# Kernel tuning notes

Hardware: AMD Instinct MI355X
Metric: run time of the kernel (lower is better)

Reference implementation:

```python
import jax, jax.numpy as jnp
import numpy as np

NEG_SLOPE = 0.2

def setup_inputs() -> dict:
    key = jax.random.key(0)
    k1, k2, k3, k4 = jax.random.split(key, 4)
    B, N, Fin, H, Fo = 8, 2000, 128, 4, 64
    x = jax.random.normal(k1, (B, N, Fin), dtype=jnp.float32)
    adj = jax.random.randint(k2, (N, N), 0, 2, dtype=jnp.int32)
    W = jax.random.normal(k3, (Fin, H * Fo), dtype=jnp.float32) * (1.0 / np.sqrt(Fin))
    a = jax.random.normal(k4, (H, 2 * Fo), dtype=jnp.float32) * 0.1
    return {"x": x, "adj": adj, "W": W, "a": a}

def reference(x, adj, W, a):
    B, N, _ = x.shape
    H, F2 = a.shape
    Fo = F2 // 2
    h = (x @ W).reshape(B, N, H, Fo)  # [B,N,H,Fo]
    # cat([h_i,h_j])*a summed over 2Fo decomposes into per-node src/dst scores
    a_src, a_dst = a[:, :Fo], a[:, Fo:]
    e_i = jnp.einsum('bnhf,hf->bnh', h, a_src)  # source (query) contribution
    e_j = jnp.einsum('bnhf,hf->bnh', h, a_dst)  # target (key) contribution
    e = jax.nn.leaky_relu(e_i[:, :, None, :] + e_j[:, None, :, :], NEG_SLOPE)  # [B,N,N,H]
    mask = (adj == 0)[None, :, :, None]
    e = jnp.where(mask, -jnp.inf, e)
    alpha = jax.nn.softmax(e, axis=2)  # softmax over neighbors j
    # dropout is identity in eval mode
    out = jnp.einsum('bijh,bjhf->bihf', alpha, h).mean(axis=2)  # [B,N,Fo]
    return out, alpha
```

## Files before the change

kernel.cpp:

```cpp
#include <hip/hip_runtime.h>
#include <math.h>

#define BB 8
#define NN 2000
#define FIN 128
#define HH 4
#define FO 64
#define CC 256

typedef short bf16x8 __attribute__((ext_vector_type(8)));
typedef float f32x4 __attribute__((ext_vector_type(4)));
typedef unsigned long long u64;

__device__ __forceinline__ unsigned short f2bf(float v) {
    union { float f; unsigned u; } x;
    x.f = v;
    unsigned r = x.u + 0x7fffu + ((x.u >> 16) & 1u);
    return (unsigned short)(r >> 16);
}

__global__ __launch_bounds__(256) void k_adjbits(const int* __restrict__ adj,
                                                 u64* __restrict__ adjb) {
    const int w = blockIdx.x * 4 + (threadIdx.x >> 6);
    const int lane = threadIdx.x & 63;
    const int i = w >> 5, wd = w & 31;
    const int j = wd * 64 + lane;
    int av = 0;
    if (j < NN) av = adj[(size_t)i * NN + j];
    const u64 mask = __ballot(av != 0);
    if (lane == 0) adjb[(size_t)i * 32 + wd] = mask;
}

__global__ __launch_bounds__(256) void k_gemm_fused(const float* __restrict__ x,
                                                    const float* __restrict__ W,
                                                    const float* __restrict__ a,
                                                    float* __restrict__ e_src,
                                                    float* __restrict__ e_dst,
                                                    unsigned short* __restrict__ hT) {
    __shared__ __align__(16) char smraw[8192];
    float* xs = (float*)smraw;
    unsigned short* sm = (unsigned short*)smraw;
    const int row0 = blockIdx.x * 16;
    const int t = threadIdx.x;
    for (int k = t; k < 16 * FIN; k += 256) xs[k] = x[row0 * FIN + k];
    __syncthreads();
    const int c = t;
    const int h = c >> 6, f = c & 63, lane = t & 63;
    float acc[16];
#pragma unroll
    for (int r = 0; r < 16; ++r) acc[r] = 0.f;
#pragma unroll 2
    for (int k = 0; k < FIN; k += 4) {
        const float w0 = W[(k + 0) * CC + c];
        const float w1 = W[(k + 1) * CC + c];
        const float w2 = W[(k + 2) * CC + c];
        const float w3 = W[(k + 3) * CC + c];
#pragma unroll
        for (int r = 0; r < 16; ++r) {
            const float4 xv = *(const float4*)(xs + r * FIN + k);
            acc[r] = fmaf(xv.x, w0, fmaf(xv.y, w1, fmaf(xv.z, w2, fmaf(xv.w, w3, acc[r]))));
        }
    }
    const int b = row0 / NN;
    const int n0 = row0 - b * NN;
    const float aS = a[h * 2 * FO + f];
    const float aD = a[h * 2 * FO + FO + f];
#pragma unroll
    for (int r = 0; r < 16; ++r) {
        float p1 = acc[r] * aS;
        float p2 = acc[r] * aD;
#pragma unroll
        for (int off = 32; off > 0; off >>= 1) {
            p1 += __shfl_xor(p1, off);
            p2 += __shfl_xor(p2, off);
        }
        if (lane == 0) {
            e_src[(b * HH + h) * NN + n0 + r] = p1;
            e_dst[(b * HH + h) * NN + n0 + r] = p2;
        }
    }
    __syncthreads();
#pragma unroll
    for (int r = 0; r < 16; ++r) sm[r * 256 + c] = f2bf(acc[r]);
    __syncthreads();
    const int s = n0 >> 5;
    const int qbase = (n0 >> 3) & 3;
    unsigned short* base = hT + (size_t)b * HH * 131072 + s * 2048;
#pragma unroll
    for (int it2 = 0; it2 < 2; ++it2) {
        const int k2 = it2 * 256 + t;
        const int hh = (k2 >> 7) & 3, ft2 = (k2 >> 5) & 3, l16 = (k2 >> 1) & 15, g = k2 & 1;
        const int col = hh * 64 + ft2 * 16 + l16;
        unsigned v[4];
#pragma unroll
        for (int p = 0; p < 4; ++p) {
            const unsigned lo = sm[(g * 8 + 2 * p) * 256 + col];
            const unsigned hi = sm[(g * 8 + 2 * p + 1) * 256 + col];
            v[p] = lo | (hi << 16);
        }
        uint4 pkt; pkt.x = v[0]; pkt.y = v[1]; pkt.z = v[2]; pkt.w = v[3];
        *(uint4*)(base + (size_t)hh * 131072 + ft2 * 512 + (qbase + g) * 128 + l16 * 8) = pkt;
    }
}

__global__ __launch_bounds__(256) void k_padT(unsigned short* __restrict__ hT) {
    const int k = blockIdx.x * 256 + threadIdx.x;
    const int bh = k / 384;
    const int r = k - bh * 384;
    const int ft = r / 96;
    const int c = r - ft * 96;
    size_t off;
    if (c < 32) off = 62 * 2048 + ft * 512 + 256 + c * 8;
    else        off = 63 * 2048 + ft * 512 + (size_t)(c - 32) * 8;
    uint4 z; z.x = 0; z.y = 0; z.z = 0; z.w = 0;
    *(uint4*)(hT + (size_t)bh * 131072 + off) = z;
}

__global__ __launch_bounds__(256) void k_softmax_l(const u64* __restrict__ adjb,
                                                   const float* __restrict__ e_src,
                                                   const float* __restrict__ e_dst,
                                                   float* __restrict__ rlArr) {
    const int widx = blockIdx.x * 4 + (threadIdx.x >> 6);
    const int lane = threadIdx.x & 63;
    const int b = widx / (NN * HH);
    const int rem = widx - b * (NN * HH);
    const int i = rem / HH;
    const int h = rem - i * HH;
    const float* ed = e_dst + (b * HH + h) * NN;
    const u64* ab = adjb + (size_t)i * 32;
    const float ei = e_src[(b * HH + h) * NN + i];
    float l = 0.f;
#pragma unroll 2
    for (int it = 0; it < 8; ++it) {
        const int j = it * 256 + lane * 4;
        const u64 wbits = ab[j >> 6];
        const unsigned nib = (unsigned)((wbits >> (j & 63)) & 0xFull);
        const float4 ev = *(const float4*)(ed + j);
        float s0 = ei + ev.x; s0 = s0 > 0.f ? s0 : 0.2f * s0;
        float s1 = ei + ev.y; s1 = s1 > 0.f ? s1 : 0.2f * s1;
        float s2 = ei + ev.z; s2 = s2 > 0.f ? s2 : 0.2f * s2;
        float s3 = ei + ev.w; s3 = s3 > 0.f ? s3 : 0.2f * s3;
        const float q0 = (nib & 1u) ? __expf(s0) : 0.f;
        const float q1 = (nib & 2u) ? __expf(s1) : 0.f;
        const float q2 = (nib & 4u) ? __expf(s2) : 0.f;
        const float q3 = (nib & 8u) ? __expf(s3) : 0.f;
        l += (q0 + q1) + (q2 + q3);
    }
#pragma unroll
    for (int off = 32; off > 0; off >>= 1) l += __shfl_xor(l, off);
    if (lane == 0) rlArr[(b * HH + h) * NN + i] = 1.f / l;
}

__global__ __launch_bounds__(512) void k_out_mfma4(const u64* __restrict__ adjb,
                                                   const unsigned short* __restrict__ hT,
                                                   const float* __restrict__ e_src,
                                                   const float* __restrict__ e_dst,
                                                   const float* __restrict__ rlArr,
                                                   float* __restrict__ out) {
    __shared__ float red[32][72];
    const int blk = blockIdx.x;
    const int b = blk / 63;
    const int it = blk - b * 63;
    const int t = threadIdx.x;
    const int w = t >> 6, lane = t & 63;
    const int h = w >> 1, half = w & 1;
    const int l16 = lane & 15, quad = lane >> 4;
    const int i = it * 32 + half * 16 + l16;
    const int ic = i < NN ? i : NN - 1;
    const int bh = b * HH + h;
    const float es = e_src[bh * NN + ic];
    const float rl = (i < NN) ? rlArr[bh * NN + ic] : 0.f;
    const float* ed = e_dst + bh * NN;
    const u64* ab = adjb + (size_t)ic * 32;
    const unsigned short* hbase = hT + (size_t)bh * 131072 + (size_t)lane * 8;

    f32x4 acc[4];
#pragma unroll
    for (int ft = 0; ft < 4; ++ft) {
        acc[ft][0] = 0.f; acc[ft][1] = 0.f; acc[ft][2] = 0.f; acc[ft][3] = 0.f;
    }

#pragma unroll 2
    for (int jt = 0; jt < 32; ++jt) {
        const int j0 = jt * 64;
        const u64 bits = ab[jt];
        const unsigned m0 = ((unsigned)(bits >> (quad * 8))) & 0xffu;
        const unsigned m1 = ((unsigned)(bits >> 32) >> (quad * 8)) & 0xffu;
        const float4 ea0 = *(const float4*)(ed + j0 + quad * 8);
        const float4 ea1 = *(const float4*)(ed + j0 + quad * 8 + 4);
        const float4 eb0 = *(const float4*)(ed + j0 + 32 + quad * 8);
        const float4 eb1 = *(const float4*)(ed + j0 + 32 + quad * 8 + 4);
        const unsigned short* hp0 = hbase + (size_t)jt * 4096;

        {
            const float ev[8] = {ea0.x, ea0.y, ea0.z, ea0.w, ea1.x, ea1.y, ea1.z, ea1.w};
            bf16x8 bfr;
#pragma unroll
            for (int e = 0; e < 8; ++e) {
                float s = es + ev[e];
                s = s > 0.f ? s : 0.2f * s;
                float p = __expf(s) * rl;
                p = ((m0 >> e) & 1u) ? p : 0.f;
                bfr[e] = (short)f2bf(p);
            }
#pragma unroll
            for (int ft = 0; ft < 4; ++ft) {
                const bf16x8 af = *(const bf16x8*)(hp0 + ft * 512);
                acc[ft] = __builtin_amdgcn_mfma_f32_16x16x32_bf16(af, bfr, acc[ft], 0, 0, 0);
            }
        }
        {
            const float ev[8] = {eb0.x, eb0.y, eb0.z, eb0.w, eb1.x, eb1.y, eb1.z, eb1.w};
            bf16x8 bfr;
#pragma unroll
            for (int e = 0; e < 8; ++e) {
                float s = es + ev[e];
                s = s > 0.f ? s : 0.2f * s;
                float p = __expf(s) * rl;
                p = ((m1 >> e) & 1u) ? p : 0.f;
                bfr[e] = (short)f2bf(p);
            }
#pragma unroll
            for (int ft = 0; ft < 4; ++ft) {
                const bf16x8 af = *(const bf16x8*)(hp0 + 2048 + ft * 512);
                acc[ft] = __builtin_amdgcn_mfma_f32_16x16x32_bf16(af, bfr, acc[ft], 0, 0, 0);
            }
        }
    }
#pragma unroll
    for (int ph = 0; ph < HH; ++ph) {
        if (h == ph) {
            if (ph == 0) {
#pragma unroll
                for (int ft = 0; ft < 4; ++ft)
                    *(f32x4*)(&red[half * 16 + l16][ft * 16 + quad * 4]) = acc[ft];
            } else {
#pragma unroll
                for (int ft = 0; ft < 4; ++ft) {
                    f32x4 cur = *(const f32x4*)(&red[half * 16 + l16][ft * 16 + quad * 4]);
#pragma unroll
                    for (int r = 0; r < 4; ++r) cur[r] += acc[ft][r];
                    *(f32x4*)(&red[half * 16 + l16][ft * 16 + quad * 4]) = cur;
                }
            }
        }
        __syncthreads();
    }
    const int ii = t >> 4, f4 = (t & 15) * 4;
    const int gi = it * 32 + ii;
    if (gi < NN) {
        const f32x4 v = *(const f32x4*)(&red[ii][f4]);
        f32x4 o;
#pragma unroll
        for (int r = 0; r < 4; ++r) o[r] = 0.25f * v[r];
        *(f32x4*)(out + (size_t)(b * NN + gi) * FO + f4) = o;
    }
}

__global__ __launch_bounds__(256) void k_alpha_bits(const u64* __restrict__ adjb,
                                                    const float* __restrict__ e_src,
                                                    const float* __restrict__ e_dst,
                                                    const float* __restrict__ rlArr,
                                                    float* __restrict__ alpha) {
    const int bi = blockIdx.x;
    const int b = bi / NN, i = bi - b * NN;
    const int t = threadIdx.x;
    float ei[HH], rr[HH];
#pragma unroll
    for (int h = 0; h < HH; ++h) {
        ei[h] = e_src[(b * HH + h) * NN + i];
        rr[h] = rlArr[(b * HH + h) * NN + i];
    }
    const float* ed = e_dst + b * HH * NN;
    const u64* ab = adjb + (size_t)i * 32;
    float* arow = alpha + (size_t)(b * NN + i) * (NN * HH);
    for (int jq = t; jq < NN / 4; jq += 256) {
        const int j0 = jq * 4;
        const unsigned bits4 = (unsigned)((ab[j0 >> 6] >> (j0 & 63)) & 0xFull);
        float e4[HH * 4];
#pragma unroll
        for (int h = 0; h < HH; ++h) {
            const float4 v = *(const float4*)(ed + h * NN + j0);
            e4[h * 4 + 0] = v.x; e4[h * 4 + 1] = v.y; e4[h * 4 + 2] = v.z; e4[h * 4 + 3] = v.w;
        }
#pragma unroll
        for (int jj = 0; jj < 4; ++jj) {
            const bool av = (bits4 >> jj) & 1u;
            float o[HH];
#pragma unroll
            for (int h = 0; h < HH; ++h) {
                float s = ei[h] + e4[h * 4 + jj];
                s = s > 0.f ? s : 0.2f * s;
                o[h] = av ? __expf(s) * rr[h] : 0.f;
            }
            float4 ov = {o[0], o[1], o[2], o[3]};
            *(float4*)(arow + (size_t)(j0 + jj) * HH) = ov;
        }
    }
}

__global__ __launch_bounds__(256) void k_alpha_adj(const int* __restrict__ adj,
                                                   const float* __restrict__ e_src,
                                                   const float* __restrict__ e_dst,
                                                   const float* __restrict__ rlArr,
                                                   float* __restrict__ alpha) {
    const int bi = blockIdx.x;
    const int b = bi / NN, i = bi - b * NN;
    const int t = threadIdx.x;
    float ei[HH], rr[HH];
#pragma unroll
    for (int h = 0; h < HH; ++h) {
        ei[h] = e_src[(b * HH + h) * NN + i];
        rr[h] = rlArr[(b * HH + h) * NN + i];
    }
    const float* ed = e_dst + b * HH * NN;
    const int* adjrow = adj + (size_t)i * NN;
    float* arow = alpha + (size_t)(b * NN + i) * (NN * HH);
    for (int jq = t; jq < NN / 4; jq += 256) {
        const int j0 = jq * 4;
        const int4 av4 = *(const int4*)(adjrow + j0);
        const int avs[4] = {av4.x, av4.y, av4.z, av4.w};
        float e4[HH * 4];
#pragma unroll
        for (int h = 0; h < HH; ++h) {
            const float4 v = *(const float4*)(ed + h * NN + j0);
            e4[h * 4 + 0] = v.x; e4[h * 4 + 1] = v.y; e4[h * 4 + 2] = v.z; e4[h * 4 + 3] = v.w;
        }
#pragma unroll
        for (int jj = 0; jj < 4; ++jj) {
            const bool av = avs[jj] != 0;
            float o[HH];
#pragma unroll
            for (int h = 0; h < HH; ++h) {
                float s = ei[h] + e4[h * 4 + jj];
                s = s > 0.f ? s : 0.2f * s;
                o[h] = av ? __expf(s) * rr[h] : 0.f;
            }
            float4 ov = {o[0], o[1], o[2], o[3]};
            *(float4*)(arow + (size_t)(j0 + jj) * HH) = ov;
        }
    }
}

extern "C" void kernel_launch(void* const* d_in, const int* in_sizes, int n_in,
                              void* d_out, int out_size, void* d_ws, size_t ws_size,
                              hipStream_t stream) {
    const float* x  = (const float*)d_in[0];
    const int* adj  = (const int*)d_in[1];
    const float* W  = (const float*)d_in[2];
    const float* a  = (const float*)d_in[3];

    float* out = (float*)d_out;
    float* alpha = out + (size_t)BB * NN * FO;

    unsigned short* hT = (unsigned short*)alpha;
    u64* adjb_scratch = (u64*)((char*)alpha + 8388608);

    char* ws = (char*)d_ws;
    float* e_src = (float*)ws;
    float* e_dst = (float*)(ws + 256000);
    float* rlArr = (float*)(ws + 512000);
    const bool ws_has_adjb = ws_size >= 1280000;
    u64* adjb = ws_has_adjb ? (u64*)(ws + 768000) : adjb_scratch;

    k_adjbits<<<16000, 256, 0, stream>>>(adj, adjb);
    k_gemm_fused<<<1000, 256, 0, stream>>>(x, W, a, e_src, e_dst, hT);
    k_padT<<<48, 256, 0, stream>>>(hT);
    k_softmax_l<<<16000, 256, 0, stream>>>(adjb, e_src, e_dst, rlArr);
    k_out_mfma4<<<504, 512, 0, stream>>>(adjb, hT, e_src, e_dst, rlArr, out);
    if (ws_has_adjb)
        k_alpha_bits<<<16000, 256, 0, stream>>>(adjb, e_src, e_dst, rlArr, alpha);
    else
        k_alpha_adj<<<16000, 256, 0, stream>>>(adj, e_src, e_dst, rlArr, alpha);
}
```

Baseline: 763.0 us.

## Fuse softmax denominator into MFMA aggregation kernel and merge adjacency/pad kernels

Removes the separate softmax row-sum kernel. The aggregation kernel now accumulates unnormalized exp weights, reduces the per-row sum across quads, rescales the accumulators and writes rlArr for the later alpha kernel. The adjacency bit-packing and hT padding kernels are merged into one launch with a grid-stride loop. The aggregation kernel also stages e_dst in shared memory, uses 256-thread blocks of 16 rows, and drops the bounds checks since 2000 divides by 16. This saves a pass over the adjacency bits and two launches. In exchange, bf16 rounding now applies to unnormalized exponentials, which could overflow or lose precision for large scores.

```diff
diff --git a/kernel.cpp b/kernel.cpp
--- a/kernel.cpp
+++ b/kernel.cpp
@@ -19,16 +19,31 @@
     return (unsigned short)(r >> 16);
 }
 
-__global__ __launch_bounds__(256) void k_adjbits(const int* __restrict__ adj,
-                                                 u64* __restrict__ adjb) {
-    const int w = blockIdx.x * 4 + (threadIdx.x >> 6);
-    const int lane = threadIdx.x & 63;
-    const int i = w >> 5, wd = w & 31;
-    const int j = wd * 64 + lane;
-    int av = 0;
-    if (j < NN) av = adj[(size_t)i * NN + j];
-    const u64 mask = __ballot(av != 0);
-    if (lane == 0) adjb[(size_t)i * 32 + wd] = mask;
+__global__ __launch_bounds__(256) void k_adjpad(const int* __restrict__ adj,
+                                                u64* __restrict__ adjb,
+                                                unsigned short* __restrict__ hT) {
+    if (blockIdx.x < 1000) {
+        const int lane = threadIdx.x & 63;
+        for (int w = blockIdx.x * 4 + (threadIdx.x >> 6); w < 64000; w += 4000) {
+            const int i = w >> 5, wd = w & 31;
+            const int j = wd * 64 + lane;
+            int av = 0;
+            if (j < NN) av = adj[(size_t)i * NN + j];
+            const u64 mask = __ballot(av != 0);
+            if (lane == 0) adjb[(size_t)i * 32 + wd] = mask;
+        }
+    } else {
+        const int k = (blockIdx.x - 1000) * 256 + threadIdx.x;
+        const int bh = k / 384;
+        const int r = k - bh * 384;
+        const int ft = r / 96;
+        const int c = r - ft * 96;
+        size_t off;
+        if (c < 32) off = 62 * 2048 + ft * 512 + 256 + c * 8;
+        else        off = 63 * 2048 + ft * 512 + (size_t)(c - 32) * 8;
+        uint4 z; z.x = 0; z.y = 0; z.z = 0; z.w = 0;
+        *(uint4*)(hT + (size_t)bh * 131072 + off) = z;
+    }
 }
 
 __global__ __launch_bounds__(256) void k_gemm_fused(const float* __restrict__ x,
@@ -103,75 +118,31 @@
     }
 }
 
-__global__ __launch_bounds__(256) void k_padT(unsigned short* __restrict__ hT) {
-    const int k = blockIdx.x * 256 + threadIdx.x;
-    const int bh = k / 384;
-    const int r = k - bh * 384;
-    const int ft = r / 96;
-    const int c = r - ft * 96;
-    size_t off;
-    if (c < 32) off = 62 * 2048 + ft * 512 + 256 + c * 8;
-    else        off = 63 * 2048 + ft * 512 + (size_t)(c - 32) * 8;
-    uint4 z; z.x = 0; z.y = 0; z.z = 0; z.w = 0;
-    *(uint4*)(hT + (size_t)bh * 131072 + off) = z;
-}
-
-__global__ __launch_bounds__(256) void k_softmax_l(const u64* __restrict__ adjb,
-                                                   const float* __restrict__ e_src,
-                                                   const float* __restrict__ e_dst,
-                                                   float* __restrict__ rlArr) {
-    const int widx = blockIdx.x * 4 + (threadIdx.x >> 6);
-    const int lane = threadIdx.x & 63;
-    const int b = widx / (NN * HH);
-    const int rem = widx - b * (NN * HH);
-    const int i = rem / HH;
-    const int h = rem - i * HH;
-    const float* ed = e_dst + (b * HH + h) * NN;
-    const u64* ab = adjb + (size_t)i * 32;
-    const float ei = e_src[(b * HH + h) * NN + i];
-    float l = 0.f;
-#pragma unroll 2
-    for (int it = 0; it < 8; ++it) {
-        const int j = it * 256 + lane * 4;
-        const u64 wbits = ab[j >> 6];
-        const unsigned nib = (unsigned)((wbits >> (j & 63)) & 0xFull);
-        const float4 ev = *(const float4*)(ed + j);
-        float s0 = ei + ev.x; s0 = s0 > 0.f ? s0 : 0.2f * s0;
-        float s1 = ei + ev.y; s1 = s1 > 0.f ? s1 : 0.2f * s1;
-        float s2 = ei + ev.z; s2 = s2 > 0.f ? s2 : 0.2f * s2;
-        float s3 = ei + ev.w; s3 = s3 > 0.f ? s3 : 0.2f * s3;
-        const float q0 = (nib & 1u) ? __expf(s0) : 0.f;
-        const float q1 = (nib & 2u) ? __expf(s1) : 0.f;
-        const float q2 = (nib & 4u) ? __expf(s2) : 0.f;
-        const float q3 = (nib & 8u) ? __expf(s3) : 0.f;
-        l += (q0 + q1) + (q2 + q3);
-    }
-#pragma unroll
-    for (int off = 32; off > 0; off >>= 1) l += __shfl_xor(l, off);
-    if (lane == 0) rlArr[(b * HH + h) * NN + i] = 1.f / l;
-}
-
-__global__ __launch_bounds__(512) void k_out_mfma4(const u64* __restrict__ adjb,
+__global__ __launch_bounds__(256) void k_out_mfma5(const u64* __restrict__ adjb,
                                                    const unsigned short* __restrict__ hT,
                                                    const float* __restrict__ e_src,
                                                    const float* __restrict__ e_dst,
-                                                   const float* __restrict__ rlArr,
+                                                   float* __restrict__ rlArr,
                                                    float* __restrict__ out) {
-    __shared__ float red[32][72];
+    __shared__ __align__(16) float eds[HH][2048];
     const int blk = blockIdx.x;
-    const int b = blk / 63;
-    const int it = blk - b * 63;
+    const int b = blk / 125;
+    const int it = blk - b * 125;
+    const int i0 = it * 16;
     const int t = threadIdx.x;
-    const int w = t >> 6, lane = t & 63;
-    const int h = w >> 1, half = w & 1;
+    const int h = t >> 6, lane = t & 63;
     const int l16 = lane & 15, quad = lane >> 4;
-    const int i = it * 32 + half * 16 + l16;
-    const int ic = i < NN ? i : NN - 1;
+    for (int idx = t; idx < 2048; idx += 256) {
+        const int h2 = idx >> 9, j4 = (idx & 511) * 4;
+        float4 v = {0.f, 0.f, 0.f, 0.f};
+        if (j4 < NN) v = *(const float4*)(e_dst + (b * HH + h2) * NN + j4);
+        *(float4*)(&eds[h2][j4]) = v;
+    }
+    __syncthreads();
+    const int i = i0 + l16;
     const int bh = b * HH + h;
-    const float es = e_src[bh * NN + ic];
-    const float rl = (i < NN) ? rlArr[bh * NN + ic] : 0.f;
-    const float* ed = e_dst + bh * NN;
-    const u64* ab = adjb + (size_t)ic * 32;
+    const float es = e_src[bh * NN + i];
+    const u64* ab = adjb + (size_t)i * 32;
     const unsigned short* hbase = hT + (size_t)bh * 131072 + (size_t)lane * 8;
 
     f32x4 acc[4];
@@ -179,28 +150,29 @@
     for (int ft = 0; ft < 4; ++ft) {
         acc[ft][0] = 0.f; acc[ft][1] = 0.f; acc[ft][2] = 0.f; acc[ft][3] = 0.f;
     }
+    float psum = 0.f;
 
 #pragma unroll 2
     for (int jt = 0; jt < 32; ++jt) {
-        const int j0 = jt * 64;
         const u64 bits = ab[jt];
         const unsigned m0 = ((unsigned)(bits >> (quad * 8))) & 0xffu;
         const unsigned m1 = ((unsigned)(bits >> 32) >> (quad * 8)) & 0xffu;
-        const float4 ea0 = *(const float4*)(ed + j0 + quad * 8);
-        const float4 ea1 = *(const float4*)(ed + j0 + quad * 8 + 4);
-        const float4 eb0 = *(const float4*)(ed + j0 + 32 + quad * 8);
-        const float4 eb1 = *(const float4*)(ed + j0 + 32 + quad * 8 + 4);
+        const float* ep = &eds[h][jt * 64 + quad * 8];
+        const f32x4 ea0 = *(const f32x4*)(ep);
+        const f32x4 ea1 = *(const f32x4*)(ep + 4);
+        const f32x4 eb0 = *(const f32x4*)(ep + 32);
+        const f32x4 eb1 = *(const f32x4*)(ep + 36);
         const unsigned short* hp0 = hbase + (size_t)jt * 4096;
 
         {
-            const float ev[8] = {ea0.x, ea0.y, ea0.z, ea0.w, ea1.x, ea1.y, ea1.z, ea1.w};
+            const float ev[8] = {ea0[0], ea0[1], ea0[2], ea0[3], ea1[0], ea1[1], ea1[2], ea1[3]};
             bf16x8 bfr;
 #pragma unroll
             for (int e = 0; e < 8; ++e) {
                 float s = es + ev[e];
                 s = s > 0.f ? s : 0.2f * s;
-                float p = __expf(s) * rl;
-                p = ((m0 >> e) & 1u) ? p : 0.f;
+                float p = ((m0 >> e) & 1u) ? __expf(s) : 0.f;
+                psum += p;
                 bfr[e] = (short)f2bf(p);
             }
 #pragma unroll
@@ -210,14 +182,14 @@
             }
         }
         {
-            const float ev[8] = {eb0.x, eb0.y, eb0.z, eb0.w, eb1.x, eb1.y, eb1.z, eb1.w};
+            const float ev[8] = {eb0[0], eb0[1], eb0[2], eb0[3], eb1[0], eb1[1], eb1[2], eb1[3]};
             bf16x8 bfr;
 #pragma unroll
             for (int e = 0; e < 8; ++e) {
                 float s = es + ev[e];
                 s = s > 0.f ? s : 0.2f * s;
-                float p = __expf(s) * rl;
-                p = ((m1 >> e) & 1u) ? p : 0.f;
+                float p = ((m1 >> e) & 1u) ? __expf(s) : 0.f;
+                psum += p;
                 bfr[e] = (short)f2bf(p);
             }
 #pragma unroll
@@ -227,34 +199,42 @@
             }
         }
     }
+    psum += __shfl_xor(psum, 16);
+    psum += __shfl_xor(psum, 32);
+    const float rl = 1.f / psum;
+#pragma unroll
+    for (int ft = 0; ft < 4; ++ft)
+#pragma unroll
+        for (int r = 0; r < 4; ++r) acc[ft][r] *= rl;
+    if (quad == 0) rlArr[bh * NN + i] = rl;
+
+    __syncthreads();
+    float* red = (float*)eds;
 #pragma unroll
     for (int ph = 0; ph < HH; ++ph) {
         if (h == ph) {
             if (ph == 0) {
 #pragma unroll
                 for (int ft = 0; ft < 4; ++ft)
-                    *(f32x4*)(&red[half * 16 + l16][ft * 16 + quad * 4]) = acc[ft];
+                    *(f32x4*)(&red[l16 * 68 + ft * 16 + quad * 4]) = acc[ft];
             } else {
 #pragma unroll
                 for (int ft = 0; ft < 4; ++ft) {
-                    f32x4 cur = *(const f32x4*)(&red[half * 16 + l16][ft * 16 + quad * 4]);
+                    f32x4 cur = *(const f32x4*)(&red[l16 * 68 + ft * 16 + quad * 4]);
 #pragma unroll
                     for (int r = 0; r < 4; ++r) cur[r] += acc[ft][r];
-                    *(f32x4*)(&red[half * 16 + l16][ft * 16 + quad * 4]) = cur;
+                    *(f32x4*)(&red[l16 * 68 + ft * 16 + quad * 4]) = cur;
                 }
             }
         }
         __syncthreads();
     }
     const int ii = t >> 4, f4 = (t & 15) * 4;
-    const int gi = it * 32 + ii;
-    if (gi < NN) {
-        const f32x4 v = *(const f32x4*)(&red[ii][f4]);
-        f32x4 o;
-#pragma unroll
-        for (int r = 0; r < 4; ++r) o[r] = 0.25f * v[r];
-        *(f32x4*)(out + (size_t)(b * NN + gi) * FO + f4) = o;
-    }
+    const f32x4 v = *(const f32x4*)(&red[ii * 68 + f4]);
+    f32x4 o;
+#pragma unroll
+    for (int r = 0; r < 4; ++r) o[r] = 0.25f * v[r];
+    *(f32x4*)(out + (size_t)(b * NN + i0 + ii) * FO + f4) = o;
 }
 
 __global__ __launch_bounds__(256) void k_alpha_bits(const u64* __restrict__ adjb,
@@ -363,11 +343,9 @@
     const bool ws_has_adjb = ws_size >= 1280000;
     u64* adjb = ws_has_adjb ? (u64*)(ws + 768000) : adjb_scratch;
 
-    k_adjbits<<<16000, 256, 0, stream>>>(adj, adjb);
+    k_adjpad<<<1048, 256, 0, stream>>>(adj, adjb, hT);
     k_gemm_fused<<<1000, 256, 0, stream>>>(x, W, a, e_src, e_dst, hT);
-    k_padT<<<48, 256, 0, stream>>>(hT);
-    k_softmax_l<<<16000, 256, 0, stream>>>(adjb, e_src, e_dst, rlArr);
-    k_out_mfma4<<<504, 512, 0, stream>>>(adjb, hT, e_src, e_dst, rlArr, out);
+    k_out_mfma5<<<1000, 256, 0, stream>>>(adjb, hT, e_src, e_dst, rlArr, out);
     if (ws_has_adjb)
         k_alpha_bits<<<16000, 256, 0, stream>>>(adjb, e_src, e_dst, rlArr, alpha);
     else
```

After: 692.8 us. 9.2% less time.
